# Kernel tuning notes

Measured on AMD Instinct MI355X. Metric: run time of the kernel, lower is better.

Reference implementation:

```python
import jax, jax.numpy as jnp
import numpy as np
from jax import lax

B, L, D = 2, 4096, 2048
K, KQ, M, H = 32, 4, 8, 8  # H = D*expand // (K*M)
MEM = K * H              # 256
FLAT = K * H * M         # 2048
CONV_W = 4
DIM_SWIGLU = H * 3 * 2   # out_expand_factor=3 -> 48
N_DECAY = K - 4          # 28 decay heads, 4 anchor heads


def setup_inputs() -> dict:
    key = jax.random.key(0)
    ks = jax.random.split(key, 8)
    x = jax.random.normal(ks[0], (B, L, D), dtype=jnp.float32)
    W_mem = jax.random.normal(ks[1], (D, MEM + K), dtype=jnp.float32) / np.sqrt(D)
    conv_k = jax.random.normal(ks[2], (CONV_W, 1, MEM + K), dtype=jnp.float32) * 0.3
    W_q = jax.random.normal(ks[3], (D, KQ * H * M * 2), dtype=jnp.float32) / np.sqrt(D)
    theta = jnp.asarray(np.tile(np.geomspace(0.001, 3.0, M).reshape(1, 1, 1, 1, M),
                                (1, 1, K, H, 1)), dtype=jnp.float32)
    decay_slopes = jnp.asarray(np.log(np.expm1(np.geomspace(0.001, 0.1, N_DECAY))), dtype=jnp.float32)
    anchor_slopes = jnp.asarray(np.log(np.expm1(np.geomspace(0.01, 0.1, 4))), dtype=jnp.float32)
    score_scale = jnp.ones((K,), dtype=jnp.float32)
    g = np.sqrt(2.0 / (H + DIM_SWIGLU))
    W_re = jax.random.normal(ks[4], (K, H, DIM_SWIGLU), dtype=jnp.float32) * g
    W_im = jax.random.normal(ks[5], (K, H, DIM_SWIGLU), dtype=jnp.float32) * g
    norm_scale = jnp.ones((1, 1, K, H), dtype=jnp.float32)
    W_out = jax.random.normal(ks[6], (K * H * 3, D), dtype=jnp.float32) / np.sqrt(K * H * 3)
    return {"x": x, "W_mem": W_mem, "conv_k": conv_k, "W_q": W_q, "theta": theta,
            "decay_slopes": decay_slopes, "anchor_slopes": anchor_slopes,
            "score_scale": score_scale, "W_re": W_re, "W_im": W_im,
            "norm_scale": norm_scale, "W_out": W_out}


def _forward(x, W_mem, conv_k, W_q, theta, decay_slopes, anchor_slopes,
             score_scale, W_re, W_im, norm_scale, W_out):
    b, l, d = x.shape
    # memory branch: dense + causal depthwise conv
    z = x @ W_mem  # (b, l, MEM+K)
    z = lax.conv_general_dilated(z, conv_k, window_strides=(1,),
                                 padding=[(CONV_W - 1, 0)],
                                 dimension_numbers=('NHC', 'HIO', 'NHC'),
                                 feature_group_count=MEM + K)
    k_val = z[..., :MEM].reshape(b, l, K, H)
    s_raw = z[..., MEM:].reshape(b, l, K, 1)
    # query branch
    q = (x @ W_q).reshape(b, l, KQ, H, M, 2)
    q_re, q_im = q[..., 0], q[..., 1]
    # per-head time weights (decay heads look back from end, anchor heads from start)
    pos = jnp.arange(l, dtype=jnp.float32)
    slopes_d = jax.nn.softplus(decay_slopes).reshape(1, 1, -1, 1)
    slopes_a = jax.nn.softplus(anchor_slopes).reshape(1, 1, -1, 1)
    dist = jnp.maximum(jnp.float32(l - 1) - pos, 0.0)
    log_w = jnp.concatenate([-slopes_d * dist[None, :, None, None],
                             -slopes_a * pos[None, :, None, None]], axis=2)  # (1,l,K,1)
    log_p = jnp.clip(score_scale[None, None, :, None] * s_raw, -20.0, 20.0)
    p_w = jnp.exp(log_p + log_w)  # (b,l,K,1)
    # complex rotation of keys
    phi = k_val[..., None] * theta          # (b,l,K,H,M)
    re_k, im_k = jnp.cos(phi), jnp.sin(phi)
    pw5 = p_w[..., None]
    merged = jnp.concatenate([p_w.squeeze(-1),
                              (pw5 * re_k).reshape(b, l, FLAT),
                              (pw5 * im_k).reshape(b, l, FLAT)], axis=-1)
    cs = jnp.cumsum(merged, axis=1)
    den = cs[..., :K]                       # (b,l,K)
    num_re = cs[..., K:K + FLAT]
    num_im = cs[..., K + FLAT:]
    inv_den = 1.0 / jnp.maximum(den[..., None], 1e-4)  # (b,l,K,1)
    state_re = num_re.reshape(b, l, K, H, M) * inv_den[..., None]
    state_im = num_im.reshape(b, l, K, H, M) * inv_den[..., None]
    # GQA-style query repeat
    n_rep = K // KQ
    q_re = jnp.repeat(q_re, n_rep, axis=2)
    q_im = jnp.repeat(q_im, n_rep, axis=2)
    out_re = jnp.sum(state_re * q_re + state_im * q_im, axis=-1)  # (b,l,K,H)
    out_im = jnp.sum(state_im * q_re - state_re * q_im, axis=-1)
    out_re = out_re * norm_scale
    out_im = out_im * norm_scale
    y = jnp.einsum('blkh,khn->blkn', out_re, W_re) + jnp.einsum('blkh,khn->blkn', out_im, W_im)
    y_val, y_gate = jnp.split(y, 2, axis=-1)
    y = (y_val * jax.nn.silu(y_gate)).reshape(b, l, -1)
    return y @ W_out


def reference(x, W_mem, conv_k, W_q, theta, decay_slopes, anchor_slopes,
              score_scale, W_re, W_im, norm_scale, W_out):
    return _forward(x, W_mem, conv_k, W_q, theta, decay_slopes, anchor_slopes,
                    score_scale, W_re, W_im, norm_scale, W_out)
```

## Files before the change

### kernel.cpp

```cpp
#include <hip/hip_runtime.h>
#include <hip/hip_bf16.h>
#include <math.h>

#define BB 2
#define LL 4096
#define DD 2048
#define KK 32
#define MEM 256
#define CTOT 288
#define NQ 512
#define ZSTR 800
#define NPAD 896
#define FLAT 2048
#define CMERG 4128
#define CH 16
#define NCH 256
#define YDIM 768
#define BL (BB*LL)

typedef __attribute__((ext_vector_type(4))) float f32x4;
typedef __attribute__((ext_vector_type(8))) short bf16x8;
typedef __attribute__((ext_vector_type(8))) unsigned short u16x8;

__device__ inline unsigned short f2b(float v) {
    __hip_bfloat16 h = __float2bfloat16(v);
    return *reinterpret_cast<unsigned short*>(&h);
}
__device__ inline float b2f(unsigned short u) {
    __hip_bfloat16 h;
    *reinterpret_cast<unsigned short*>(&h) = u;
    return __bfloat162float(h);
}

__device__ inline void gload16(const void* g, void* l) {
    __builtin_amdgcn_global_load_lds(
        (const __attribute__((address_space(1))) unsigned int*)g,
        (__attribute__((address_space(3))) unsigned int*)l, 16, 0, 0);
}

__device__ inline void wait_stage(int it, int nIter) {
    if (it + 3 <= nIter) asm volatile("s_waitcnt vmcnt(8)" ::: "memory");
    else if (it + 2 == nIter) asm volatile("s_waitcnt vmcnt(4)" ::: "memory");
    else asm volatile("s_waitcnt vmcnt(0)" ::: "memory");
}

template<int HH>
__device__ inline float bcast8(float v) {
    return __int_as_float(__builtin_amdgcn_ds_swizzle(__float_as_int(v), (HH << 5) | 0x18));
}

__device__ inline float fast_sigmoid_mul(float val, float g) {
    return val * __builtin_amdgcn_rcpf(1.f + __expf(-g));
}

__global__ __launch_bounds__(256) void cvt_x(const float* __restrict__ x,
                                             unsigned short* __restrict__ xb) {
    size_t i = ((size_t)blockIdx.x * 256 + threadIdx.x) * 8;
    float4 a = *(const float4*)&x[i];
    float4 b = *(const float4*)&x[i + 4];
    u16x8 o;
    o[0] = f2b(a.x); o[1] = f2b(a.y); o[2] = f2b(a.z); o[3] = f2b(a.w);
    o[4] = f2b(b.x); o[5] = f2b(b.y); o[6] = f2b(b.z); o[7] = f2b(b.w);
    *(u16x8*)&xb[i] = o;
}

__global__ __launch_bounds__(256) void prep_wb(const float* __restrict__ W_mem,
                                               const float* __restrict__ W_q,
                                               unsigned short* __restrict__ Wb) {
    int n = blockIdx.x;
    for (int k = threadIdx.x; k < DD; k += 256) {
        float v = 0.f;
        if (n < CTOT) v = W_mem[(size_t)k * CTOT + n];
        else if (n < ZSTR) v = W_q[(size_t)k * NQ + (n - CTOT)];
        Wb[(size_t)n * DD + k] = f2b(v);
    }
}

__global__ __launch_bounds__(256) void prep_wo(const float* __restrict__ W_out,
                                               unsigned short* __restrict__ Wo) {
    int n = blockIdx.x;
    for (int k = threadIdx.x; k < YDIM; k += 256) {
        Wo[(size_t)n * YDIM + k] = f2b(W_out[(size_t)k * DD + n]);
    }
}

template<bool CBF16>
__global__ __launch_bounds__(256) void gemm_mfma(const unsigned short* __restrict__ A,
                                                 const unsigned short* __restrict__ Bh_g,
                                                 void* __restrict__ Cout,
                                                 int Kd, int Nvalid, int Cstride) {
    __shared__ unsigned short As[4][4096];
    __shared__ unsigned short Bh[4][4096];
    int tid = threadIdx.x;
    int lane = tid & 63;
    int wave = tid >> 6;
    int wr = wave >> 1, wc = wave & 1;

    int nwg = gridDim.x * gridDim.y;
    int bid = blockIdx.y * gridDim.x + blockIdx.x;
    int cpx = nwg >> 3;
    int swz = (bid & 7) * cpx + (bid >> 3);
    int bx = swz % gridDim.x, by = swz / gridDim.x;
    int m0 = by * 128;
    int n0 = bx * 128;

    f32x4 acc[4][4];
#pragma unroll
    for (int i = 0; i < 4; ++i)
#pragma unroll
        for (int j = 0; j < 4; ++j) acc[i][j] = (f32x4){0.f, 0.f, 0.f, 0.f};

    int f0 = tid, f1 = 256 + tid;
    int row0 = f0 >> 2, ks0 = (f0 & 3) ^ ((row0 >> 1) & 3);
    int row1 = f1 >> 2, ks1 = (f1 & 3) ^ ((row1 >> 1) & 3);
    const unsigned short* ga0 = &A[(size_t)(m0 + row0) * Kd + ks0 * 8];
    const unsigned short* ga1 = &A[(size_t)(m0 + row1) * Kd + ks1 * 8];
    const unsigned short* gb0 = &Bh_g[(size_t)(n0 + row0) * Kd + ks0 * 8];
    const unsigned short* gb1 = &Bh_g[(size_t)(n0 + row1) * Kd + ks1 * 8];
    int l0 = (wave * 64) * 8;
    int l1 = (256 + wave * 64) * 8;

    int g = lane >> 4, rr = lane & 15;

#define STAGE(buf, koff) do {                                          \
        gload16(ga0 + (koff), &As[buf][l0]);                           \
        gload16(ga1 + (koff), &As[buf][l1]);                           \
        gload16(gb0 + (koff), &Bh[buf][l0]);                           \
        gload16(gb1 + (koff), &Bh[buf][l1]);                           \
    } while (0)

    int nIter = Kd >> 5;
    STAGE(0, 0);
    STAGE(1, 32);

    for (int it = 0; it < nIter; ++it) {
        int cur = it & 3;
        if (it + 2 < nIter) STAGE((it + 2) & 3, (it + 2) * 32);
        wait_stage(it, nIter);
        __builtin_amdgcn_s_barrier();

        bf16x8 av[4], bhv[4];
#pragma unroll
        for (int i = 0; i < 4; ++i) {
            int ra = wr * 64 + i * 16 + rr;
            av[i] = *(const bf16x8*)&As[cur][ra * 32 + ((g ^ ((ra >> 1) & 3)) * 8)];
            int rb = wc * 64 + i * 16 + rr;
            bhv[i] = *(const bf16x8*)&Bh[cur][rb * 32 + ((g ^ ((rb >> 1) & 3)) * 8)];
        }
#pragma unroll
        for (int i = 0; i < 4; ++i)
#pragma unroll
            for (int j = 0; j < 4; ++j)
                acc[i][j] = __builtin_amdgcn_mfma_f32_16x16x32_bf16(av[i], bhv[j], acc[i][j], 0, 0, 0);
    }
#undef STAGE

    int cg = lane >> 4, cr = lane & 15;
#pragma unroll
    for (int i = 0; i < 4; ++i)
#pragma unroll
        for (int j = 0; j < 4; ++j) {
            int colb = n0 + wc * 64 + j * 16 + cr;
            if (colb < Nvalid) {
#pragma unroll
                for (int r = 0; r < 4; ++r) {
                    int rowb = m0 + wr * 64 + i * 16 + cg * 4 + r;
                    if (CBF16)
                        ((unsigned short*)Cout)[(size_t)rowb * Cstride + colb] = f2b(acc[i][j][r]);
                    else
                        ((float*)Cout)[(size_t)rowb * Cstride + colb] = acc[i][j][r];
                }
            }
        }
}

__global__ __launch_bounds__(512, 2) void gemm256(const unsigned short* __restrict__ A,
                                                  const unsigned short* __restrict__ Bm,
                                                  float* __restrict__ C,
                                                  int Kd, int Cstride) {
    __shared__ __attribute__((aligned(16))) unsigned short As[4][8192];
    __shared__ __attribute__((aligned(16))) unsigned short Bs[4][8192];
    int tid = threadIdx.x;
    int lane = tid & 63, wave = tid >> 6;
    int wm = wave >> 2, wn = wave & 3;

    int nwg = gridDim.x * gridDim.y;
    int bid = blockIdx.y * gridDim.x + blockIdx.x;
    int cpx = nwg >> 3;
    int swz = (bid & 7) * cpx + (bid >> 3);
    int bx = swz % gridDim.x, by = swz / gridDim.x;
    int m0 = by * 256, n0 = bx * 256;

    f32x4 acc[8][4];
#pragma unroll
    for (int i = 0; i < 8; ++i)
#pragma unroll
        for (int j = 0; j < 4; ++j) acc[i][j] = (f32x4){0.f, 0.f, 0.f, 0.f};

    const unsigned short* pA[2];
    const unsigned short* pB[2];
    int ldsoff[2];
#pragma unroll
    for (int j = 0; j < 2; ++j) {
        int f = j * 512 + tid;
        int row = f >> 2, s = f & 3;
        int sg = s ^ ((row >> 1) & 3);
        pA[j] = A + (size_t)(m0 + row) * Kd + sg * 8;
        pB[j] = Bm + (size_t)(n0 + row) * Kd + sg * 8;
        ldsoff[j] = (j * 512 + wave * 64) * 8;
    }

    int rr = lane & 15, kg = lane >> 4;

#define STAGE(buf, koff) do {                                          \
        gload16(pA[0] + (koff), &As[buf][ldsoff[0]]);                  \
        gload16(pA[1] + (koff), &As[buf][ldsoff[1]]);                  \
        gload16(pB[0] + (koff), &Bs[buf][ldsoff[0]]);                  \
        gload16(pB[1] + (koff), &Bs[buf][ldsoff[1]]);                  \
    } while (0)

    int nT = Kd >> 5;
    STAGE(0, 0);
    STAGE(1, 32);

#define LDA(fr) ({ int ra_ = wm * 128 + (fr) * 16 + rr;                          \
        *(const bf16x8*)&As[cur][ra_ * 32 + ((kg ^ ((ra_ >> 1) & 3)) * 8)]; })
#define LDB(fc) ({ int rb_ = wn * 64 + (fc) * 16 + rr;                           \
        *(const bf16x8*)&Bs[cur][rb_ * 32 + ((kg ^ ((rb_ >> 1) & 3)) * 8)]; })

    for (int it = 0; it < nT; ++it) {
        int cur = it & 3;
        if (it + 2 < nT) STAGE((it + 2) & 3, (it + 2) * 32);
        wait_stage(it, nT);
        __builtin_amdgcn_s_barrier();

        bf16x8 bv[4];
#pragma unroll
        for (int j = 0; j < 4; ++j) bv[j] = LDB(j);
#pragma unroll
        for (int i = 0; i < 8; ++i) {
            bf16x8 a0 = LDA(i);
#pragma unroll
            for (int j = 0; j < 4; ++j)
                acc[i][j] = __builtin_amdgcn_mfma_f32_16x16x32_bf16(a0, bv[j], acc[i][j], 0, 0, 0);
        }
    }
#undef LDA
#undef LDB
#undef STAGE

    int cg = lane >> 4;
#pragma unroll
    for (int i = 0; i < 8; ++i)
#pragma unroll
        for (int j = 0; j < 4; ++j) {
            int colb = n0 + wn * 64 + j * 16 + rr;
#pragma unroll
            for (int r = 0; r < 4; ++r) {
                int rowb = m0 + wm * 128 + i * 16 + cg * 4 + r;
                C[(size_t)rowb * Cstride + colb] = acc[i][j][r];
            }
        }
}

__global__ __launch_bounds__(256) void fused_partial(const unsigned short* __restrict__ zq,
                                                     const float* __restrict__ conv_k,
                                                     const float* __restrict__ theta,
                                                     const float* __restrict__ decay,
                                                     const float* __restrict__ anchor,
                                                     const float* __restrict__ sscale,
                                                     float* __restrict__ partials) {
    int chunk = blockIdx.x, b = blockIdx.y, t = threadIdx.x;
    int l0 = chunk * CH;
    __shared__ unsigned short zin[CH + 3][CTOT];

    for (int idx = t; idx < (CH + 3) * 36; idx += 256) {
        int r = idx / 36, c8 = (idx % 36) * 8;
        int l = l0 - 3 + r;
        u16x8 v = (u16x8)(0);
        if (l >= 0) v = *(const u16x8*)&zq[(size_t)(b * LL + l) * ZSTR + c8];
        *(u16x8*)&zin[r][c8] = v;
    }
    __syncthreads();

    int k = t >> 3;
    float cz0 = conv_k[t], cz1 = conv_k[CTOT + t], cz2 = conv_k[2 * CTOT + t], cz3 = conv_k[3 * CTOT + t];
    int sc = MEM + k;
    float cs0 = conv_k[sc], cs1 = conv_k[CTOT + sc], cs2 = conv_k[2 * CTOT + sc], cs3 = conv_k[3 * CTOT + sc];
    float xx = (k < KK - 4) ? decay[k] : anchor[k - (KK - 4)];
    float sp = (xx > 20.f) ? xx : log1pf(__expf(xx));
    float ss = sscale[k];
    float th[8];
#pragma unroll
    for (int m = 0; m < 8; ++m) th[m] = theta[t * 8 + m];
    float rs[8], is[8];
#pragma unroll
    for (int m = 0; m < 8; ++m) { rs[m] = 0.f; is[m] = 0.f; }
    float dsum = 0.f;

#pragma unroll 1
    for (int i = 0; i < CH; ++i) {
        float kv = b2f(zin[i][t]) * cz0 + b2f(zin[i + 1][t]) * cz1 +
                   b2f(zin[i + 2][t]) * cz2 + b2f(zin[i + 3][t]) * cz3;
        float s = b2f(zin[i][sc]) * cs0 + b2f(zin[i + 1][sc]) * cs1 +
                  b2f(zin[i + 2][sc]) * cs2 + b2f(zin[i + 3][sc]) * cs3;
        int l = l0 + i;
        float lw = (k < KK - 4) ? -sp * (float)(LL - 1 - l) : -sp * (float)l;
        float lp = fminf(fmaxf(ss * s, -20.f), 20.f);
        float p = __expf(lp + lw);
        dsum += p;
#pragma unroll
        for (int m = 0; m < 8; ++m) {
            float sn, cn;
            __sincosf(kv * th[m], &sn, &cn);
            rs[m] += p * cn;
            is[m] += p * sn;
        }
    }
    size_t base = ((size_t)b * NCH + chunk) * CMERG;
    *(f32x4*)&partials[base + KK + t * 8]            = (f32x4){rs[0], rs[1], rs[2], rs[3]};
    *(f32x4*)&partials[base + KK + t * 8 + 4]        = (f32x4){rs[4], rs[5], rs[6], rs[7]};
    *(f32x4*)&partials[base + KK + FLAT + t * 8]     = (f32x4){is[0], is[1], is[2], is[3]};
    *(f32x4*)&partials[base + KK + FLAT + t * 8 + 4] = (f32x4){is[4], is[5], is[6], is[7]};
    if ((t & 7) == 0) partials[base + k] = dsum;
}

__global__ __launch_bounds__(256) void scan_partials(float* __restrict__ partials) {
    int t = threadIdx.x;
    int cl = t & 15, j = t >> 4;
    int c = blockIdx.x * 16 + cl;
    int b = blockIdx.y;
    float v[16];
    float s = 0.f;
#pragma unroll
    for (int i = 0; i < 16; ++i) {
        v[i] = partials[((size_t)b * NCH + j * 16 + i) * CMERG + c];
        s += v[i];
    }
    __shared__ float sums[16][17];
    sums[j][cl] = s;
    __syncthreads();
    if (j == 0) {
        float run = 0.f;
#pragma unroll
        for (int jj = 0; jj < 16; ++jj) {
            float x = sums[jj][cl];
            sums[jj][cl] = run;
            run += x;
        }
    }
    __syncthreads();
    float run = sums[j][cl];
#pragma unroll
    for (int i = 0; i < 16; ++i) {
        float x = v[i];
        partials[((size_t)b * NCH + j * 16 + i) * CMERG + c] = run;
        run += x;
    }
}

__global__ __launch_bounds__(256) void fused_stage(const unsigned short* __restrict__ zq,
                                                   const float* __restrict__ conv_k,
                                                   const float* __restrict__ theta,
                                                   const float* __restrict__ decay,
                                                   const float* __restrict__ anchor,
                                                   const float* __restrict__ sscale,
                                                   const float* __restrict__ partials,
                                                   const float* __restrict__ W_re,
                                                   const float* __restrict__ W_im,
                                                   const float* __restrict__ nscale,
                                                   unsigned short* __restrict__ y_act) {
    int chunk = blockIdx.x, b = blockIdx.y, t = threadIdx.x;
    int l0 = chunk * CH;
    __shared__ unsigned short zin[CH + 3][CTOT];
    __shared__ unsigned short qall[CH][NQ];

    for (int idx = t; idx < (CH + 3) * 36; idx += 256) {
        int r = idx / 36, c8 = (idx % 36) * 8;
        int l = l0 - 3 + r;
        u16x8 v = (u16x8)(0);
        if (l >= 0) v = *(const u16x8*)&zq[(size_t)(b * LL + l) * ZSTR + c8];
        *(u16x8*)&zin[r][c8] = v;
    }
    for (int idx = t; idx < CH * (NQ / 8); idx += 256) {
        int i = idx >> 6, c8 = (idx & 63) * 8;
        *(u16x8*)&qall[i][c8] = *(const u16x8*)&zq[(size_t)(b * LL + l0 + i) * ZSTR + CTOT + c8];
    }
    __syncthreads();

    int k = t >> 3, h = t & 7, w = t >> 6;
    float cz0 = conv_k[t], cz1 = conv_k[CTOT + t], cz2 = conv_k[2 * CTOT + t], cz3 = conv_k[3 * CTOT + t];
    int sc = MEM + k;
    float cs0 = conv_k[sc], cs1 = conv_k[CTOT + sc], cs2 = conv_k[2 * CTOT + sc], cs3 = conv_k[3 * CTOT + sc];
    float xx = (k < KK - 4) ? decay[k] : anchor[k - (KK - 4)];
    float sp = (xx > 20.f) ? xx : log1pf(__expf(xx));
    float ss = sscale[k];
    float th[8];
#pragma unroll
    for (int m = 0; m < 8; ++m) th[m] = theta[t * 8 + m];
    float ns = nscale[t];
    int qb = w * 128 + h * 16;

    float wre[8][6], wim[8][6];
#pragma unroll
    for (int hh = 0; hh < 8; ++hh)
#pragma unroll
        for (int jj = 0; jj < 6; ++jj) {
            wre[hh][jj] = W_re[(k * 8 + hh) * 48 + h + 8 * jj];
            wim[hh][jj] = W_im[(k * 8 + hh) * 48 + h + 8 * jj];
        }

    size_t pbase = ((size_t)b * NCH + chunk) * CMERG;
    f32x4 r0 = *(const f32x4*)&partials[pbase + KK + t * 8];
    f32x4 r1 = *(const f32x4*)&partials[pbase + KK + t * 8 + 4];
    f32x4 i0 = *(const f32x4*)&partials[pbase + KK + FLAT + t * 8];
    f32x4 i1 = *(const f32x4*)&partials[pbase + KK + FLAT + t * 8 + 4];
    float rs[8] = {r0[0], r0[1], r0[2], r0[3], r1[0], r1[1], r1[2], r1[3]};
    float is[8] = {i0[0], i0[1], i0[2], i0[3], i1[0], i1[1], i1[2], i1[3]};
    float den = partials[pbase + k];

#pragma unroll 1
    for (int i = 0; i < CH; ++i) {
        float kv = b2f(zin[i][t]) * cz0 + b2f(zin[i + 1][t]) * cz1 +
                   b2f(zin[i + 2][t]) * cz2 + b2f(zin[i + 3][t]) * cz3;
        float s = b2f(zin[i][sc]) * cs0 + b2f(zin[i + 1][sc]) * cs1 +
                  b2f(zin[i + 2][sc]) * cs2 + b2f(zin[i + 3][sc]) * cs3;
        int l = l0 + i;
        float lw = (k < KK - 4) ? -sp * (float)(LL - 1 - l) : -sp * (float)l;
        float lp = fminf(fmaxf(ss * s, -20.f), 20.f);
        float p = __expf(lp + lw);
        den += p;
        float inv = __builtin_amdgcn_rcpf(fmaxf(den, 1e-4f));
#pragma unroll
        for (int m = 0; m < 8; ++m) {
            float sn, cn;
            __sincosf(kv * th[m], &sn, &cn);
            rs[m] += p * cn;
            is[m] += p * sn;
        }
        u16x8 qv0 = *(const u16x8*)&qall[i][qb];
        u16x8 qv1 = *(const u16x8*)&qall[i][qb + 8];
        float o_re = 0.f, o_im = 0.f;
#pragma unroll
        for (int m = 0; m < 8; ++m) {
            float sre = rs[m] * inv;
            float sim = is[m] * inv;
            float qre = b2f((unsigned short)((m < 4) ? qv0[2 * m] : qv1[2 * m - 8]));
            float qim = b2f((unsigned short)((m < 4) ? qv0[2 * m + 1] : qv1[2 * m - 7]));
            o_re += sre * qre + sim * qim;
            o_im += sim * qre - sre * qim;
        }
        o_re *= ns;
        o_im *= ns;

        float y0 = 0.f, y1 = 0.f, y2 = 0.f, y3 = 0.f, y4 = 0.f, y5 = 0.f;
#define EAPPLY(HH) { float br_ = bcast8<HH>(o_re); float bi_ = bcast8<HH>(o_im); \
        y0 += br_ * wre[HH][0] + bi_ * wim[HH][0]; \
        y1 += br_ * wre[HH][1] + bi_ * wim[HH][1]; \
        y2 += br_ * wre[HH][2] + bi_ * wim[HH][2]; \
        y3 += br_ * wre[HH][3] + bi_ * wim[HH][3]; \
        y4 += br_ * wre[HH][4] + bi_ * wim[HH][4]; \
        y5 += br_ * wre[HH][5] + bi_ * wim[HH][5]; }
        EAPPLY(0) EAPPLY(1) EAPPLY(2) EAPPLY(3)
        EAPPLY(4) EAPPLY(5) EAPPLY(6) EAPPLY(7)
#undef EAPPLY

        size_t ybase = (size_t)(b * LL + l) * YDIM + k * 24 + h;
        y_act[ybase]      = f2b(fast_sigmoid_mul(y0 * y3, y3));
        y_act[ybase + 8]  = f2b(fast_sigmoid_mul(y1 * y4, y4));
        y_act[ybase + 16] = f2b(fast_sigmoid_mul(y2 * y5, y5));
    }
}

extern "C" void kernel_launch(void* const* d_in, const int* in_sizes, int n_in,
                              void* d_out, int out_size, void* d_ws, size_t ws_size,
                              hipStream_t stream) {
    const float* x      = (const float*)d_in[0];
    const float* W_mem  = (const float*)d_in[1];
    const float* conv_k = (const float*)d_in[2];
    const float* W_q    = (const float*)d_in[3];
    const float* theta  = (const float*)d_in[4];
    const float* decay  = (const float*)d_in[5];
    const float* anchor = (const float*)d_in[6];
    const float* sscale = (const float*)d_in[7];
    const float* W_re   = (const float*)d_in[8];
    const float* W_im   = (const float*)d_in[9];
    const float* nscale = (const float*)d_in[10];
    const float* W_out  = (const float*)d_in[11];
    float* out = (float*)d_out;
    float* ws = (float*)d_ws;

    unsigned short* xb = (unsigned short*)out;
    unsigned short* Wb = (unsigned short*)(out + 8388608);
    unsigned short* zq = (unsigned short*)(out + 9306112);
    float* partials      = ws;
    unsigned short* yb   = (unsigned short*)(ws + 2113536);
    unsigned short* Wo   = (unsigned short*)(ws + 5259264);

    cvt_x<<<8192, 256, 0, stream>>>(x, xb);
    prep_wb<<<NPAD, 256, 0, stream>>>(W_mem, W_q, Wb);
    prep_wo<<<DD, 256, 0, stream>>>(W_out, Wo);

    gemm_mfma<true><<<dim3(NPAD / 128, BL / 128), 256, 0, stream>>>(
        xb, Wb, zq, DD, ZSTR, ZSTR);
    fused_partial<<<dim3(NCH, BB), 256, 0, stream>>>(zq, conv_k, theta, decay, anchor, sscale, partials);
    scan_partials<<<dim3(CMERG / 16, BB), 256, 0, stream>>>(partials);
    fused_stage<<<dim3(NCH, BB), 256, 0, stream>>>(zq, conv_k, theta, decay, anchor, sscale,
                                                   partials, W_re, W_im, nscale, yb);
    gemm256<<<dim3(DD / 256, BL / 256), 512, 0, stream>>>(yb, Wo, out, YDIM, DD);
}
```

Before: 161.4 us.

## Fuse fp32-to-bf16 conversion of x into the first GEMM's LDS load path

Removes the separate cvt_x kernel and has the input projection GEMM load x directly in fp32 into LDS, converting to bf16 when building MFMA operands. This avoids writing and re-reading a bf16 copy of x and drops one launch. In exchange the A tile takes twice the LDS and global load bandwidth per stage, each wave repeats the conversion for tiles it shares, and the pipeline goes from four-stage buffering with fine-grained vmcnt waits to double buffering with full __syncthreads, which may expose more load latency.

```diff
diff --git a/kernel.cpp b/kernel.cpp
--- a/kernel.cpp
+++ b/kernel.cpp
@@ -53,17 +53,6 @@
     return val * __builtin_amdgcn_rcpf(1.f + __expf(-g));
 }
 
-__global__ __launch_bounds__(256) void cvt_x(const float* __restrict__ x,
-                                             unsigned short* __restrict__ xb) {
-    size_t i = ((size_t)blockIdx.x * 256 + threadIdx.x) * 8;
-    float4 a = *(const float4*)&x[i];
-    float4 b = *(const float4*)&x[i + 4];
-    u16x8 o;
-    o[0] = f2b(a.x); o[1] = f2b(a.y); o[2] = f2b(a.z); o[3] = f2b(a.w);
-    o[4] = f2b(b.x); o[5] = f2b(b.y); o[6] = f2b(b.z); o[7] = f2b(b.w);
-    *(u16x8*)&xb[i] = o;
-}
-
 __global__ __launch_bounds__(256) void prep_wb(const float* __restrict__ W_mem,
                                                const float* __restrict__ W_q,
                                                unsigned short* __restrict__ Wb) {
@@ -84,13 +73,12 @@
     }
 }
 
-template<bool CBF16>
-__global__ __launch_bounds__(256) void gemm_mfma(const unsigned short* __restrict__ A,
-                                                 const unsigned short* __restrict__ Bh_g,
-                                                 void* __restrict__ Cout,
-                                                 int Kd, int Nvalid, int Cstride) {
-    __shared__ unsigned short As[4][4096];
-    __shared__ unsigned short Bh[4][4096];
+__global__ __launch_bounds__(256) void gemm_zq(const float* __restrict__ Af,
+                                               const unsigned short* __restrict__ Bh_g,
+                                               unsigned short* __restrict__ Cout,
+                                               int Kd, int Nvalid, int Cstride) {
+    __shared__ __attribute__((aligned(16))) float As[2][4096];
+    __shared__ __attribute__((aligned(16))) unsigned short Bh[2][4096];
     int tid = threadIdx.x;
     int lane = tid & 63;
     int wave = tid >> 6;
@@ -110,40 +98,56 @@
 #pragma unroll
         for (int j = 0; j < 4; ++j) acc[i][j] = (f32x4){0.f, 0.f, 0.f, 0.f};
 
-    int f0 = tid, f1 = 256 + tid;
-    int row0 = f0 >> 2, ks0 = (f0 & 3) ^ ((row0 >> 1) & 3);
-    int row1 = f1 >> 2, ks1 = (f1 & 3) ^ ((row1 >> 1) & 3);
-    const unsigned short* ga0 = &A[(size_t)(m0 + row0) * Kd + ks0 * 8];
-    const unsigned short* ga1 = &A[(size_t)(m0 + row1) * Kd + ks1 * 8];
-    const unsigned short* gb0 = &Bh_g[(size_t)(n0 + row0) * Kd + ks0 * 8];
-    const unsigned short* gb1 = &Bh_g[(size_t)(n0 + row1) * Kd + ks1 * 8];
-    int l0 = (wave * 64) * 8;
-    int l1 = (256 + wave * 64) * 8;
+    const float* pA[4];
+    int offA[4];
+#pragma unroll
+    for (int j = 0; j < 4; ++j) {
+        int f = j * 256 + tid;
+        int row = f >> 3, s = f & 7;
+        int sg = s ^ (row & 7);
+        pA[j] = Af + (size_t)(m0 + row) * Kd + sg * 4;
+        offA[j] = f * 4;
+    }
+    const unsigned short* pB[2];
+    int offB[2];
+#pragma unroll
+    for (int j = 0; j < 2; ++j) {
+        int f = j * 256 + tid;
+        int row = f >> 2, s = f & 3;
+        int sg = s ^ ((row >> 1) & 3);
+        pB[j] = Bh_g + (size_t)(n0 + row) * Kd + sg * 8;
+        offB[j] = f * 8;
+    }
 
     int g = lane >> 4, rr = lane & 15;
 
-#define STAGE(buf, koff) do {                                          \
-        gload16(ga0 + (koff), &As[buf][l0]);                           \
-        gload16(ga1 + (koff), &As[buf][l1]);                           \
-        gload16(gb0 + (koff), &Bh[buf][l0]);                           \
-        gload16(gb1 + (koff), &Bh[buf][l1]);                           \
+#define STAGE(buf, k0) do {                                            \
+        gload16(pA[0] + (k0), &As[buf][offA[0]]);                      \
+        gload16(pA[1] + (k0), &As[buf][offA[1]]);                      \
+        gload16(pA[2] + (k0), &As[buf][offA[2]]);                      \
+        gload16(pA[3] + (k0), &As[buf][offA[3]]);                      \
+        gload16(pB[0] + (k0), &Bh[buf][offB[0]]);                      \
+        gload16(pB[1] + (k0), &Bh[buf][offB[1]]);                      \
     } while (0)
 
+    STAGE(0, 0);
+    __syncthreads();
+
     int nIter = Kd >> 5;
-    STAGE(0, 0);
-    STAGE(1, 32);
-
+    int cur = 0;
     for (int it = 0; it < nIter; ++it) {
-        int cur = it & 3;
-        if (it + 2 < nIter) STAGE((it + 2) & 3, (it + 2) * 32);
-        wait_stage(it, nIter);
-        __builtin_amdgcn_s_barrier();
+        if (it + 1 < nIter) STAGE(cur ^ 1, (it + 1) * 32);
 
         bf16x8 av[4], bhv[4];
 #pragma unroll
         for (int i = 0; i < 4; ++i) {
             int ra = wr * 64 + i * 16 + rr;
-            av[i] = *(const bf16x8*)&As[cur][ra * 32 + ((g ^ ((ra >> 1) & 3)) * 8)];
+            f32x4 alo = *(const f32x4*)&As[cur][ra * 32 + ((2 * g) ^ (ra & 7)) * 4];
+            f32x4 ahi = *(const f32x4*)&As[cur][ra * 32 + ((2 * g + 1) ^ (ra & 7)) * 4];
+            u16x8 ua;
+            ua[0] = f2b(alo[0]); ua[1] = f2b(alo[1]); ua[2] = f2b(alo[2]); ua[3] = f2b(alo[3]);
+            ua[4] = f2b(ahi[0]); ua[5] = f2b(ahi[1]); ua[6] = f2b(ahi[2]); ua[7] = f2b(ahi[3]);
+            av[i] = *(bf16x8*)&ua;
             int rb = wc * 64 + i * 16 + rr;
             bhv[i] = *(const bf16x8*)&Bh[cur][rb * 32 + ((g ^ ((rb >> 1) & 3)) * 8)];
         }
@@ -152,6 +156,9 @@
 #pragma unroll
             for (int j = 0; j < 4; ++j)
                 acc[i][j] = __builtin_amdgcn_mfma_f32_16x16x32_bf16(av[i], bhv[j], acc[i][j], 0, 0, 0);
+
+        __syncthreads();
+        cur ^= 1;
     }
 #undef STAGE
 
@@ -165,10 +172,7 @@
 #pragma unroll
                 for (int r = 0; r < 4; ++r) {
                     int rowb = m0 + wr * 64 + i * 16 + cg * 4 + r;
-                    if (CBF16)
-                        ((unsigned short*)Cout)[(size_t)rowb * Cstride + colb] = f2b(acc[i][j][r]);
-                    else
-                        ((float*)Cout)[(size_t)rowb * Cstride + colb] = acc[i][j][r];
+                    Cout[(size_t)rowb * Cstride + colb] = f2b(acc[i][j][r]);
                 }
             }
         }
@@ -490,19 +494,17 @@
     float* out = (float*)d_out;
     float* ws = (float*)d_ws;
 
-    unsigned short* xb = (unsigned short*)out;
-    unsigned short* Wb = (unsigned short*)(out + 8388608);
-    unsigned short* zq = (unsigned short*)(out + 9306112);
+    unsigned short* Wb = (unsigned short*)out;
+    unsigned short* zq = (unsigned short*)(out + 917504);
     float* partials      = ws;
     unsigned short* yb   = (unsigned short*)(ws + 2113536);
     unsigned short* Wo   = (unsigned short*)(ws + 5259264);
 
-    cvt_x<<<8192, 256, 0, stream>>>(x, xb);
     prep_wb<<<NPAD, 256, 0, stream>>>(W_mem, W_q, Wb);
     prep_wo<<<DD, 256, 0, stream>>>(W_out, Wo);
 
-    gemm_mfma<true><<<dim3(NPAD / 128, BL / 128), 256, 0, stream>>>(
-        xb, Wb, zq, DD, ZSTR, ZSTR);
+    gemm_zq<<<dim3(NPAD / 128, BL / 128), 256, 0, stream>>>(
+        x, Wb, zq, DD, ZSTR, ZSTR);
     fused_partial<<<dim3(NCH, BB), 256, 0, stream>>>(zq, conv_k, theta, decay, anchor, sscale, partials);
     scan_partials<<<dim3(CMERG / 16, BB), 256, 0, stream>>>(partials);
     fused_stage<<<dim3(NCH, BB), 256, 0, stream>>>(zq, conv_k, theta, decay, anchor, sscale,
```

After: 154.5 us, median of 3. -4.3%, faster.
